# Performance work log

Measured on AMD Instinct MI355X. Metric: run time of the kernel, lower is better.

## Reference

```python
import jax, jax.numpy as jnp
import numpy as np

# Module config (defaults from __init__) and attention sizing
T, H, W = 16, 32, 32          # resolution (t, h, w)
KT, KS = 7, 7                 # window_size_t, window_size_s (dilation = 1)
HEADS, HEAD_DIM = 8, 64
C = HEADS * HEAD_DIM          # 512
B = 1                         # true batch; hidden_states leading dim = B*H*W


def nb_idx(L, K):
    """NATTEN (dilation=1) neighborhood indices: window of size K centered at i,
    shifted (clamped) at borders so it always stays in-bounds. -> [L, K] int."""
    i = jnp.arange(L)
    start = jnp.clip(i - K // 2, 0, L - K)
    return start[:, None] + jnp.arange(K)[None, :]


def setup_inputs() -> dict:
    key = jax.random.key(0)
    ks = jax.random.split(key, 5)
    x = jax.random.normal(ks[0], (B * H * W, T, C), jnp.float32)
    w_q = jax.random.normal(ks[1], (C, C), jnp.float32) * 0.02
    w_k = jax.random.normal(ks[2], (C, C), jnp.float32) * 0.02
    w_v = jax.random.normal(ks[3], (C, C), jnp.float32) * 0.02
    w_o = jax.random.normal(ks[4], (C, C), jnp.float32) * 0.02
    b_o = jnp.zeros((C,), jnp.float32)
    return {"hidden_states": x, "w_q": w_q, "w_k": w_k, "w_v": w_v,
            "w_o": w_o, "b_o": b_o}


def _attend(q, k, v):
    """3D neighborhood attention (natten3dqk + softmax + natten3dav).
    q, k, v: [b, nh, T, H, W, hd] fp32 -> out: [b, nh, T, H, W, hd].
    Scans over the KT*KS*KS = 343 window offsets so only one shifted copy of
    k / v is materialized at a time (faithful to NATTEN's locally-sparse math)."""
    t_nb, h_nb, w_nb = nb_idx(T, KT), nb_idx(H, KS), nb_idx(W, KS)
    g = jnp.meshgrid(jnp.arange(KT), jnp.arange(KS), jnp.arange(KS), indexing='ij')
    offs = tuple(a.reshape(-1) for a in g)

    def gather(x, j):
        jt, jh, jw = j
        kt, kh, kw = t_nb[:, jt], h_nb[:, jh], w_nb[:, jw]  # [T],[H],[W]
        return x[:, :, kt[:, None, None], kh[None, :, None], kw[None, None, :], :]

    @jax.checkpoint
    def qk_step(_, j):
        # raw dot product, no scaling (matches the explicit natten3dqk call)
        return None, jnp.einsum('bnthwd,bnthwd->bnthw', q, gather(k, j))

    _, qk = jax.lax.scan(qk_step, None, offs)          # [343, b, nh, T, H, W]
    ats = jax.nn.softmax(qk, axis=0)                   # softmax over neighbors

    @jax.checkpoint
    def av_step(acc, inp):
        j, a = inp                                     # a: [b, nh, T, H, W]
        return acc + a[..., None] * gather(v, j), None

    out, _ = jax.lax.scan(av_step, jnp.zeros_like(q), (offs, ats))
    return out


def reference(hidden_states, w_q, w_k, w_v, w_o, b_o):
    bhw, t, c = hidden_states.shape                    # [(b h w), T, C]
    b = bhw // (H * W)

    q = hidden_states @ w_q
    k = hidden_states @ w_k
    v = hidden_states @ w_v

    def to_heads(x):  # '(b h w) t (nh hd) -> b nh t h w hd'
        x = x.reshape(b, H, W, T, HEADS, HEAD_DIM)
        return jnp.transpose(x, (0, 4, 3, 1, 2, 5))

    q, k, v = (to_heads(x).astype(jnp.float32) for x in (q, k, v))

    out = _attend(q, k, v)                             # [b, nh, T, H, W, hd]

    # 'b nh t h w hd -> (b h w) t (nh hd)'
    out = jnp.transpose(out, (0, 3, 4, 2, 1, 5)).reshape(bhw, T, C)
    return out @ w_o + b_o                             # to_out[0]; dropout = id
```

## Files before the change

kernel.cpp:

```cpp
#include <hip/hip_runtime.h>

typedef unsigned int u32;
typedef unsigned short u16;
typedef __attribute__((ext_vector_type(8))) __bf16 bf16x8;
typedef __attribute__((ext_vector_type(4))) float f32x4;
typedef __attribute__((ext_vector_type(2))) unsigned int u32x2;

#define T_   16
#define HH   32
#define WW   32
#define HEADS_ 8
#define HD_  64
#define CC   512
#define NPOS 16384
#define CQKV 1536

__device__ __forceinline__ u16 f2bf(float f){
  u32 u = __builtin_bit_cast(u32, f);
  u32 r = u + 0x7FFFu + ((u >> 16) & 1u);
  return (u16)(r >> 16);
}

__device__ __forceinline__ u32 cvt_pk_bf16(float lo, float hi){
  u32 r;
  asm("v_cvt_pk_bf16_f32 %0, %1, %2" : "=v"(r) : "v"(lo), "v"(hi));
  return r;
}

__device__ __forceinline__ void gload16(const void* g, void* l){
  __builtin_amdgcn_global_load_lds(
    (const __attribute__((address_space(1))) void*)g,
    (__attribute__((address_space(3))) void*)l, 16, 0, 0);
}

__global__ __launch_bounds__(256) void k_convert_x(const float* __restrict__ x,
                                                   u16* __restrict__ xb){
  int i = blockIdx.x * 256 + threadIdx.x;
  const float4 a = ((const float4*)x)[i*2];
  const float4 b = ((const float4*)x)[i*2+1];
  union { u16 h[8]; uint4 q; } o;
  o.h[0]=f2bf(a.x); o.h[1]=f2bf(a.y); o.h[2]=f2bf(a.z); o.h[3]=f2bf(a.w);
  o.h[4]=f2bf(b.x); o.h[5]=f2bf(b.y); o.h[6]=f2bf(b.z); o.h[7]=f2bf(b.w);
  ((uint4*)xb)[i] = o.q;
}

__global__ __launch_bounds__(256) void k_convert_w(const float* __restrict__ wq,
                                                   const float* __restrict__ wk,
                                                   const float* __restrict__ wv,
                                                   const float* __restrict__ wo,
                                                   u16* __restrict__ wt,
                                                   u16* __restrict__ wot){
  int i = blockIdx.x * 256 + threadIdx.x;
  if (i < 1536*512){
    int n = i >> 9, k = i & 511;
    const float* src = (n < 512) ? wq : (n < 1024) ? wk : wv;
    wt[i] = f2bf(src[k*512 + (n & 511)]);
  } else {
    int j = i - 1536*512;
    int n = j >> 9, k = j & 511;
    wot[j] = f2bf(wo[k*512 + n]);
  }
}

template<int OUTMODE>
__global__ __launch_bounds__(256) void k_gemm_bt(
    const u16* __restrict__ A, const u16* __restrict__ Bt,
    void* __restrict__ C, const float* __restrict__ bias,
    int M, int N, int K)
{
  __shared__ u16 lds[2][2][128*32];
  const int tid = threadIdx.x;
  const int lane = tid & 63;
  const int l15 = lane & 15, lhi = lane >> 4;
  const int wv = tid >> 6;
  const int tm = blockIdx.y * 128, tn = blockIdx.x * 128;
  const int wm = (wv >> 1) * 64, wn = (wv & 1) * 64;
  const int nk = K >> 5;

  auto stage = [&](int buf, int kb){
    #pragma unroll
    for (int half = 0; half < 2; ++half){
      int c = tid + half*256;
      int row = c >> 2;
      int g = (c & 3) ^ ((c >> 3) & 3);
      char* la = (char*)(&lds[buf][0][0]) + ((c >> 6) << 10);
      gload16(A + (size_t)(tm + row) * K + (kb << 5) + (g << 3), la);
      char* lb = (char*)(&lds[buf][1][0]) + ((c >> 6) << 10);
      gload16(Bt + (size_t)(tn + row) * K + (kb << 5) + (g << 3), lb);
    }
  };

  stage(0, 0);
  f32x4 acc[4][4];
  const f32x4 z4 = {0.f, 0.f, 0.f, 0.f};
  #pragma unroll
  for (int i = 0; i < 4; ++i)
    #pragma unroll
    for (int j = 0; j < 4; ++j) acc[i][j] = z4;
  __syncthreads();

  int buf = 0;
  for (int kb = 0; kb < nk; ++kb){
    if (kb + 1 < nk) stage(buf ^ 1, kb + 1);
    const char* la = (const char*)(&lds[buf][0][0]);
    const char* lb = (const char*)(&lds[buf][1][0]);
    bf16x8 af[4], bfr[4];
    #pragma unroll
    for (int ai = 0; ai < 4; ++ai){
      int row = wm + ai*16 + l15;
      af[ai] = *(const bf16x8*)(la + row*64 + ((lhi ^ ((row >> 1) & 3)) << 4));
    }
    #pragma unroll
    for (int bj = 0; bj < 4; ++bj){
      int row = wn + bj*16 + l15;
      bfr[bj] = *(const bf16x8*)(lb + row*64 + ((lhi ^ ((row >> 1) & 3)) << 4));
    }
    #pragma unroll
    for (int ai = 0; ai < 4; ++ai)
      #pragma unroll
      for (int bj = 0; bj < 4; ++bj)
        acc[ai][bj] = __builtin_amdgcn_mfma_f32_16x16x32_bf16(af[ai], bfr[bj], acc[ai][bj], 0, 0, 0);
    __syncthreads();
    buf ^= 1;
  }

  #pragma unroll
  for (int ai = 0; ai < 4; ++ai)
    #pragma unroll
    for (int bj = 0; bj < 4; ++bj)
      #pragma unroll
      for (int r = 0; r < 4; ++r){
        int rr = tm + wm + ai*16 + (lhi << 2) + r;
        int cc = tn + wn + bj*16 + l15;
        float v = acc[ai][bj][r];
        if (OUTMODE == 0) ((u16*)C)[(size_t)rr * N + cc] = f2bf(v);
        else              ((float*)C)[(size_t)rr * N + cc] = v + bias[cc];
      }
}

__global__ __launch_bounds__(256) void k_vt(const u16* __restrict__ qkv,
                                            u16* __restrict__ vt){
  __shared__ u16 tl[64][65];
  const int tid = threadIdx.x;
  const int m0 = blockIdx.y << 6, c0 = blockIdx.x << 6;
  #pragma unroll
  for (int i = 0; i < 16; ++i){
    int idx = tid + (i << 8);
    int r = idx >> 6, c = idx & 63;
    tl[r][c] = qkv[(size_t)(m0 + r) * CQKV + 1024 + c0 + c];
  }
  __syncthreads();
  #pragma unroll
  for (int i = 0; i < 16; ++i){
    int idx = tid + (i << 8);
    int d = idx >> 6, mm = idx & 63;
    vt[((size_t)(c0 + d) << 14) + m0 + mm] = tl[mm][d];
  }
}

__global__ __launch_bounds__(512) void k_attn(const u16* __restrict__ qkv,
                                              const u16* __restrict__ vt,
                                              u16* __restrict__ ao){
  __shared__ u16 ldsK[2][16384];
  __shared__ u16 ldsV[2][16384];
  const int tid = threadIdx.x;
  const int lane = tid & 63;
  const int wv = tid >> 6;
  const int l15 = lane & 15, lhi = lane >> 4;
  const int bid = blockIdx.x;
  const int head = bid & 7;
  const int sp = bid >> 3;
  const int hrow = sp >> 2, wg = sp & 3;
  const int wq = (wg << 3) + wv;
  const int hw = (hrow << 5) + wq;
  const int hs = min(max(hrow - 3, 0), HH - 7);
  const int cb = min(max((wg << 3) - 3, 0), 18);
  const int offw = min(max(wq - 3, 0), WW - 7) - cb;

  const size_t qoff = ((size_t)hw * 16 + l15) * CQKV + head * HD_ + (lhi << 3);
  const bf16x8 qb0 = *(const bf16x8*)(qkv + qoff);
  const bf16x8 qb1 = *(const bf16x8*)(qkv + qoff + 32);

  const int tst = min(max(l15 - 3, 0), T_ - 7);
  bool val[4];
  #pragma unroll
  for (int r = 0; r < 4; ++r){
    int tp = (lhi << 2) + r;
    val[r] = (tp >= tst) && (tp < tst + 7);
  }

  const int srcb = l15 + ((lhi & 1) << 5);
  const bool bval = (lhi < 2);

  auto stageK = [&](int buf, int jh){
    const int hw0 = ((hs + jh) << 5) + cb;
    #pragma unroll
    for (int rnd = 0; rnd < 4; ++rnd){
      int c = tid + (rnd << 9);
      int lc = c ^ ((c >> 3) & 7);
      int s = lc >> 7, tt = (lc >> 3) & 15, ch16 = lc & 7;
      const u16* src = qkv + ((size_t)(hw0 + s) * 16 + tt) * CQKV + CC + head * HD_ + (ch16 << 3);
      gload16(src, &ldsK[buf][(size_t)((rnd << 9) + (wv << 6)) * 8]);
    }
  };
  auto stageV = [&](int buf, int jh){
    const int mb = (((hs + jh) << 5) + cb) << 4;
    #pragma unroll
    for (int rnd = 0; rnd < 4; ++rnd){
      int c = tid + (rnd << 9);
      int lc = c ^ ((c >> 5) & 7);
      int d = lc >> 5, m16 = lc & 31;
      const u16* src = vt + (((size_t)(head * HD_ + d)) << 14) + mb + (m16 << 3);
      gload16(src, &ldsV[buf][(size_t)((rnd << 9) + (wv << 6)) * 8]);
    }
  };

  float mrun = -3.0e38f, lp = 0.f;
  f32x4 oacc[4];
  const f32x4 z4 = {0.f,0.f,0.f,0.f};
  #pragma unroll
  for (int c = 0; c < 4; ++c) oacc[c] = z4;

  stageK(0, 0); stageV(0, 0);
  __syncthreads();

  int buf = 0;
  const int sw_ = (l15 & 7) << 4;
  for (int jh = 0; jh < 7; ++jh){
    if (jh < 6){ stageK(buf ^ 1, jh + 1); stageV(buf ^ 1, jh + 1); }
    const char* KB = (const char*)&ldsK[buf][0];
    const char* VB = (const char*)&ldsV[buf][0];

    f32x4 st[7];
    #pragma unroll
    for (int s = 0; s < 7; ++s){
      const int ab = ((offw + s) << 11) + (l15 << 7) + (lhi << 4);
      const bf16x8 ka0 = *(const bf16x8*)(KB + ((ab)      ^ sw_));
      const bf16x8 ka1 = *(const bf16x8*)(KB + ((ab + 64) ^ sw_));
      f32x4 acc = z4;
      acc = __builtin_amdgcn_mfma_f32_16x16x32_bf16(ka0, qb0, acc, 0, 0, 0);
      acc = __builtin_amdgcn_mfma_f32_16x16x32_bf16(ka1, qb1, acc, 0, 0, 0);
      st[s] = acc;
    }
    float tmax = -3.0e38f;
    #pragma unroll
    for (int s = 0; s < 7; ++s)
      #pragma unroll
      for (int r = 0; r < 4; ++r){
        float sv = val[r] ? st[s][r] : -1.0e30f;
        st[s][r] = sv;
        tmax = fmaxf(tmax, sv);
      }
    tmax = fmaxf(tmax, __shfl_xor(tmax, 16));
    tmax = fmaxf(tmax, __shfl_xor(tmax, 32));
    const float mnew = fmaxf(mrun, tmax);
    const float sc = __expf(mrun - mnew);
    mrun = mnew;
    lp *= sc;
    #pragma unroll
    for (int c = 0; c < 4; ++c){
      oacc[c][0] *= sc; oacc[c][1] *= sc; oacc[c][2] *= sc; oacc[c][3] *= sc;
    }
    #pragma unroll
    for (int s = 0; s < 7; ++s){
      float p0 = __expf(st[s][0] - mnew);
      float p1 = __expf(st[s][1] - mnew);
      float p2 = __expf(st[s][2] - mnew);
      float p3 = __expf(st[s][3] - mnew);
      lp += (p0 + p1) + (p2 + p3);
      u32 px = cvt_pk_bf16(p0, p1);
      u32 py = cvt_pk_bf16(p2, p3);
      u32 w0 = __shfl(px, srcb);
      u32 w1 = __shfl(py, srcb);
      u32 w2 = __shfl(px, srcb + 16);
      u32 w3 = __shfl(py, srcb + 16);
      union { u32 u[4]; bf16x8 v; } bb;
      bb.u[0] = bval ? w0 : 0u;
      bb.u[1] = bval ? w1 : 0u;
      bb.u[2] = bval ? w2 : 0u;
      bb.u[3] = bval ? w3 : 0u;
      #pragma unroll
      for (int c = 0; c < 4; ++c){
        const int d = (c << 4) + l15;
        const int vb_ = (d << 9) + ((offw + s) << 5) + (lhi << 4);
        const bf16x8 va = *(const bf16x8*)(VB + (vb_ ^ sw_));
        oacc[c] = __builtin_amdgcn_mfma_f32_16x16x32_bf16(va, bb.v, oacc[c], 0, 0, 0);
      }
    }
    __syncthreads();
    buf ^= 1;
  }

  float lsum = lp;
  lsum += __shfl_xor(lsum, 16);
  lsum += __shfl_xor(lsum, 32);
  const float inv = 1.0f / lsum;

  const size_t obase = ((size_t)hw * 16 + l15) * CC + head * HD_ + (lhi << 2);
  #pragma unroll
  for (int c = 0; c < 4; ++c){
    u32x2 o;
    o.x = cvt_pk_bf16(oacc[c][0] * inv, oacc[c][1] * inv);
    o.y = cvt_pk_bf16(oacc[c][2] * inv, oacc[c][3] * inv);
    *(u32x2*)(ao + obase + c * 16) = o;
  }
}

extern "C" void kernel_launch(void* const* d_in, const int* in_sizes, int n_in,
                              void* d_out, int out_size, void* d_ws, size_t ws_size,
                              hipStream_t stream){
  const float* x  = (const float*)d_in[0];
  const float* wq = (const float*)d_in[1];
  const float* wk = (const float*)d_in[2];
  const float* wv = (const float*)d_in[3];
  const float* wo = (const float*)d_in[4];
  const float* bo = (const float*)d_in[5];

  char* ws = (char*)d_ws;
  u16* Xb  = (u16*)(ws);
  u16* Wt  = (u16*)(ws + 16777216);
  u16* Wot = (u16*)(ws + 18350080);
  u16* QKV = (u16*)(ws + 18874368);
  u16* Vt  = (u16*)(ws + 69206016);
  u16* AO  = (u16*)(ws + 85983360);

  k_convert_x<<<4096, 256, 0, stream>>>(x, Xb);
  k_convert_w<<<4096, 256, 0, stream>>>(wq, wk, wv, wo, Wt, Wot);
  { dim3 g(12, 128); k_gemm_bt<0><<<g, 256, 0, stream>>>(Xb, Wt, QKV, nullptr, 16384, 1536, 512); }
  { dim3 g(8, 256);  k_vt<<<g, 256, 0, stream>>>(QKV, Vt); }
  k_attn<<<1024, 512, 0, stream>>>(QKV, Vt, AO);
  { dim3 g(4, 128);  k_gemm_bt<1><<<g, 256, 0, stream>>>(AO, Wot, (float*)d_out, bo, 16384, 512, 512); }
}
```

Before: 164.4 us.

## Read V directly from global memory and remap GEMM block order

The attention kernel no longer stages V tiles into LDS; each wave now loads its V fragments straight from the transposed V buffer in global memory for the AV MFMAs. This halves LDS use and adds an occupancy hint (launch_bounds 512,4) so more blocks can be resident per CU. In exchange, V reads go through the cache hierarchy without reuse across waves, which can add latency and redundant traffic. The GEMM kernel also remaps its flat block index in groups of eight, likely to spread consecutive tiles across XCDs for cache locality.

```diff
diff --git a/kernel.cpp b/kernel.cpp
--- a/kernel.cpp
+++ b/kernel.cpp
@@ -73,7 +73,11 @@
   const int lane = tid & 63;
   const int l15 = lane & 15, lhi = lane >> 4;
   const int wv = tid >> 6;
-  const int tm = blockIdx.y * 128, tn = blockIdx.x * 128;
+  const int gx = gridDim.x;
+  const int nwg = gx * gridDim.y;
+  int flat = blockIdx.y * gx + blockIdx.x;
+  flat = (flat & 7) * (nwg >> 3) + (flat >> 3);
+  const int tm = (flat / gx) * 128, tn = (flat % gx) * 128;
   const int wm = (wv >> 1) * 64, wn = (wv & 1) * 64;
   const int nk = K >> 5;
 
@@ -158,11 +162,10 @@
   }
 }
 
-__global__ __launch_bounds__(512) void k_attn(const u16* __restrict__ qkv,
-                                              const u16* __restrict__ vt,
-                                              u16* __restrict__ ao){
+__global__ __launch_bounds__(512, 4) void k_attn(const u16* __restrict__ qkv,
+                                                 const u16* __restrict__ vt,
+                                                 u16* __restrict__ ao){
   __shared__ u16 ldsK[2][16384];
-  __shared__ u16 ldsV[2][16384];
   const int tid = threadIdx.x;
   const int lane = tid & 63;
   const int wv = tid >> 6;
@@ -175,7 +178,8 @@
   const int hw = (hrow << 5) + wq;
   const int hs = min(max(hrow - 3, 0), HH - 7);
   const int cb = min(max((wg << 3) - 3, 0), 18);
-  const int offw = min(max(wq - 3, 0), WW - 7) - cb;
+  const int wsq = min(max(wq - 3, 0), WW - 7);
+  const int offw = wsq - cb;
 
   const size_t qoff = ((size_t)hw * 16 + l15) * CQKV + head * HD_ + (lhi << 3);
   const bf16x8 qb0 = *(const bf16x8*)(qkv + qoff);
@@ -203,17 +207,6 @@
       gload16(src, &ldsK[buf][(size_t)((rnd << 9) + (wv << 6)) * 8]);
     }
   };
-  auto stageV = [&](int buf, int jh){
-    const int mb = (((hs + jh) << 5) + cb) << 4;
-    #pragma unroll
-    for (int rnd = 0; rnd < 4; ++rnd){
-      int c = tid + (rnd << 9);
-      int lc = c ^ ((c >> 5) & 7);
-      int d = lc >> 5, m16 = lc & 31;
-      const u16* src = vt + (((size_t)(head * HD_ + d)) << 14) + mb + (m16 << 3);
-      gload16(src, &ldsV[buf][(size_t)((rnd << 9) + (wv << 6)) * 8]);
-    }
-  };
 
   float mrun = -3.0e38f, lp = 0.f;
   f32x4 oacc[4];
@@ -221,15 +214,15 @@
   #pragma unroll
   for (int c = 0; c < 4; ++c) oacc[c] = z4;
 
-  stageK(0, 0); stageV(0, 0);
+  stageK(0, 0);
   __syncthreads();
 
   int buf = 0;
   const int sw_ = (l15 & 7) << 4;
   for (int jh = 0; jh < 7; ++jh){
-    if (jh < 6){ stageK(buf ^ 1, jh + 1); stageV(buf ^ 1, jh + 1); }
+    if (jh < 6) stageK(buf ^ 1, jh + 1);
     const char* KB = (const char*)&ldsK[buf][0];
-    const char* VB = (const char*)&ldsV[buf][0];
+    const int rowb = ((hs + jh) << 5) + wsq;
 
     f32x4 st[7];
     #pragma unroll
@@ -279,11 +272,11 @@
       bb.u[1] = bval ? w1 : 0u;
       bb.u[2] = bval ? w2 : 0u;
       bb.u[3] = bval ? w3 : 0u;
+      const int vm = ((rowb + s) << 4) + (lhi << 3);
       #pragma unroll
       for (int c = 0; c < 4; ++c){
-        const int d = (c << 4) + l15;
-        const int vb_ = (d << 9) + ((offw + s) << 5) + (lhi << 4);
-        const bf16x8 va = *(const bf16x8*)(VB + (vb_ ^ sw_));
+        const size_t voff = ((size_t)(head * HD_ + c * 16 + l15) << 14) + vm;
+        const bf16x8 va = *(const bf16x8*)(vt + voff);
         oacc[c] = __builtin_amdgcn_mfma_f32_16x16x32_bf16(va, bb.v, oacc[c], 0, 0, 0);
       }
     }
```

Result: slower. 353.0 us (+114.8%).
